# Kernel tuning notes

Measured on AMD Instinct MI355X. Metric: run time of the kernel, lower is better.

## Reference

```python
import jax, jax.numpy as jnp
import numpy as np

UNITS = 512
EPS = 1e-6

def setup_inputs() -> dict:
    key = jax.random.key(0)
    x = jax.random.normal(key, (262144, UNITS), dtype=jnp.float32)
    return {"x": x}

def reference(x):
    d = x.shape[1]
    # Gram matrix with diagonal jitter: [d, d]
    g = x.T @ x + jnp.eye(d, dtype=x.dtype) * EPS
    L = jnp.linalg.cholesky(g)  # lower triangular [d, d]
    # inv(L) via triangular solve (same math as tf.linalg.inv on L)
    L_inv = jax.scipy.linalg.solve_triangular(L, jnp.eye(d, dtype=x.dtype), lower=True)
    ortho_weights = L_inv.T * jnp.sqrt(jnp.float32(UNITS))
    return x @ ortho_weights
```

## Files before the change

### kernel.cpp

```cpp
#include <hip/hip_runtime.h>


#define EPSJ 1e-6f
#define SQRTD 22.627416997969522f

typedef short bf16x8 __attribute__((ext_vector_type(8)));
typedef float f32x4 __attribute__((ext_vector_type(4)));

__device__ __forceinline__ unsigned short f2bf(float f) {
  unsigned u = __float_as_uint(f);
  unsigned r = u + 0x7fffu + ((u >> 16) & 1u);
  return (unsigned short)(r >> 16);
}

__device__ __forceinline__ int swz(int row, int slot) {
  return slot ^ ((row ^ (row >> 3)) & 7);
}

__device__ __forceinline__ float wred(float s) {
  s += __shfl_xor(s, 1);  s += __shfl_xor(s, 2);  s += __shfl_xor(s, 4);
  s += __shfl_xor(s, 8);  s += __shfl_xor(s, 16); s += __shfl_xor(s, 32);
  return s;
}

#define GLOAD16(g, l)                                                         \
  __builtin_amdgcn_global_load_lds(                                           \
      (const __attribute__((address_space(1))) void*)(g),                     \
      (__attribute__((address_space(3))) void*)(l), 16, 0, 0)

__global__ void convert_bf(const float* __restrict__ X,
                           unsigned short* __restrict__ Xbf) {
  long idx = (long)blockIdx.x * blockDim.x + threadIdx.x;
  const long stride = (long)gridDim.x * blockDim.x;
  const long nch = 134217728 / 8;
  for (long i = idx; i < nch; i += stride) {
    float4 f0 = ((const float4*)X)[i * 2];
    float4 f1 = ((const float4*)X)[i * 2 + 1];
    uint4 o;
    o.x = (unsigned)f2bf(f0.x) | ((unsigned)f2bf(f0.y) << 16);
    o.y = (unsigned)f2bf(f0.z) | ((unsigned)f2bf(f0.w) << 16);
    o.z = (unsigned)f2bf(f1.x) | ((unsigned)f2bf(f1.y) << 16);
    o.w = (unsigned)f2bf(f1.z) | ((unsigned)f2bf(f1.w) << 16);
    ((uint4*)Xbf)[i] = o;
  }
}

__device__ __forceinline__ void stage_pack4(
    const unsigned short* __restrict__ src,
    unsigned short* dst, int c0, int kg) {
  uint4 r0 = *(const uint4*)src;
  uint4 r1 = *(const uint4*)(src + 512);
  uint4 r2 = *(const uint4*)(src + 1024);
  uint4 r3 = *(const uint4*)(src + 1536);
  unsigned a[4] = {r0.x, r0.y, r0.z, r0.w};
  unsigned b[4] = {r1.x, r1.y, r1.z, r1.w};
  unsigned c[4] = {r2.x, r2.y, r2.z, r2.w};
  unsigned d[4] = {r3.x, r3.y, r3.z, r3.w};
  const int khi = kg >> 1, koff = (kg & 1) * 8;
  #pragma unroll
  for (int s = 0; s < 8; ++s) {
    int wsel = s >> 1, sh = (s & 1) * 16;
    unsigned v0 = (a[wsel] >> sh) & 0xFFFFu;
    unsigned v1 = (b[wsel] >> sh) & 0xFFFFu;
    unsigned v2 = (c[wsel] >> sh) & 0xFFFFu;
    unsigned v3 = (d[wsel] >> sh) & 0xFFFFu;
    int cc = c0 + s;
    int sl = khi ^ ((cc ^ (cc >> 3)) & 7);
    *(uint2*)((char*)dst + cc * 128 + sl * 16 + koff) =
        make_uint2(v0 | (v1 << 16), v2 | (v3 << 16));
  }
}

__global__ __launch_bounds__(512, 2) void gram_bf(
    const unsigned short* __restrict__ Xbf, float* __restrict__ part,
    int nchunk) {
  __shared__ unsigned short As[256 * 64];
  __shared__ unsigned short Bs[256 * 64];
  const int b = blockIdx.x, pos = b % 3, chunk = b / 3;
  const int s0 = (int)((long)4096 * chunk / nchunk);
  const int s1 = (int)((long)4096 * (chunk + 1) / nchunk);
  const int ca = (pos == 1) ? 256 : 0;
  const int cb2 = (pos == 0) ? 0 : 256;
  const bool diag = (pos != 2);
  const int t = threadIdx.x, lane = t & 63, w = t >> 6;
  const int wr = w >> 2, wc = w & 3;

  f32x4 acc[8][4];
  const f32x4 zf = {0.f, 0.f, 0.f, 0.f};
  #pragma unroll
  for (int a = 0; a < 8; ++a)
    #pragma unroll
    for (int bb = 0; bb < 4; ++bb) acc[a][bb] = zf;

  const int c0 = (t & 31) * 8;
  const int kg = t >> 5;

  for (int ks = s0; ks < s1; ++ks) {
    long r = (long)ks * 64 + kg * 4;
    stage_pack4(Xbf + r * 512 + ca + c0, As, c0, kg);
    if (!diag) stage_pack4(Xbf + r * 512 + cb2 + c0, Bs, c0, kg);
    __syncthreads();
    const unsigned short* Bp = diag ? As : Bs;
    #pragma unroll
    for (int kk = 0; kk < 2; ++kk) {
      bf16x8 af[8], bfr[4];
      #pragma unroll
      for (int fm = 0; fm < 8; ++fm) {
        int row = wr * 128 + fm * 16 + (lane & 15);
        int slot = swz(row, kk * 4 + (lane >> 4));
        af[fm] = *(const bf16x8*)((const char*)As + row * 128 + slot * 16);
      }
      #pragma unroll
      for (int fn = 0; fn < 4; ++fn) {
        int row = wc * 64 + fn * 16 + (lane & 15);
        int slot = swz(row, kk * 4 + (lane >> 4));
        bfr[fn] = *(const bf16x8*)((const char*)Bp + row * 128 + slot * 16);
      }
      #pragma unroll
      for (int fm = 0; fm < 8; ++fm)
        #pragma unroll
        for (int fn = 0; fn < 4; ++fn)
          acc[fm][fn] = __builtin_amdgcn_mfma_f32_16x16x32_bf16(
              bfr[fn], af[fm], acc[fm][fn], 0, 0, 0);
    }
    __syncthreads();
  }
  float* out = part + (long)b * 65536;
  #pragma unroll
  for (int fm = 0; fm < 8; ++fm)
    #pragma unroll
    for (int fn = 0; fn < 4; ++fn) {
      int mi = wr * 128 + fm * 16 + (lane & 15);
      int nj = wc * 64 + fn * 16 + (lane >> 4) * 4;
      *(float4*)(out + mi * 256 + nj) = *(float4*)&acc[fm][fn];
    }
}

__global__ __launch_bounds__(512, 2) void gram_f32(
    const float* __restrict__ X, float* __restrict__ part, int nchunk) {
  __shared__ unsigned short As[256 * 64];
  __shared__ unsigned short Bs[256 * 64];
  const int b = blockIdx.x;
  const int pos = b % 3;
  const int chunk = b / 3;
  const int CR = 262144 / nchunk;
  const long r0 = (long)chunk * CR;
  const int ca = (pos == 1) ? 256 : 0;
  const int cb = (pos == 0) ? 0 : 256;
  const bool diag = (pos != 2);
  const int t = threadIdx.x, lane = t & 63, w = t >> 6;
  const int wr = w >> 2, wc = w & 3;

  f32x4 acc[8][4];
  const f32x4 zf = {0.f, 0.f, 0.f, 0.f};
  #pragma unroll
  for (int a = 0; a < 8; ++a)
    #pragma unroll
    for (int bb = 0; bb < 4; ++bb) acc[a][bb] = zf;

  const int c_oct = t & 31, msub = t >> 5;

  for (int ks = 0; ks < CR; ks += 64) {
    #pragma unroll
    for (int it = 0; it < 4; ++it) {
      int m = msub + 16 * it;
      long row = r0 + ks + m;
      const float4* sa = (const float4*)(X + row * 512 + ca + c_oct * 8);
      float4 a0 = sa[0], a1 = sa[1];
      {
        float v[8] = {a0.x, a0.y, a0.z, a0.w, a1.x, a1.y, a1.z, a1.w};
        #pragma unroll
        for (int s = 0; s < 8; ++s) {
          int cc = c_oct * 8 + s;
          int off = cc * 128 + ((2 * m) ^ (((cc ^ (cc >> 3)) & 7) << 4));
          *(unsigned short*)((char*)As + off) = f2bf(v[s]);
        }
      }
      if (!diag) {
        const float4* sb = (const float4*)(X + row * 512 + cb + c_oct * 8);
        float4 b0 = sb[0], b1 = sb[1];
        float v[8] = {b0.x, b0.y, b0.z, b0.w, b1.x, b1.y, b1.z, b1.w};
        #pragma unroll
        for (int s = 0; s < 8; ++s) {
          int cc = c_oct * 8 + s;
          int off = cc * 128 + ((2 * m) ^ (((cc ^ (cc >> 3)) & 7) << 4));
          *(unsigned short*)((char*)Bs + off) = f2bf(v[s]);
        }
      }
    }
    __syncthreads();
    const unsigned short* Bp = diag ? As : Bs;
    #pragma unroll
    for (int kk = 0; kk < 2; ++kk) {
      bf16x8 af[8], bfr[4];
      #pragma unroll
      for (int fm = 0; fm < 8; ++fm) {
        int row = wr * 128 + fm * 16 + (lane & 15);
        int slot = swz(row, kk * 4 + (lane >> 4));
        af[fm] = *(const bf16x8*)((const char*)As + row * 128 + slot * 16);
      }
      #pragma unroll
      for (int fn = 0; fn < 4; ++fn) {
        int row = wc * 64 + fn * 16 + (lane & 15);
        int slot = swz(row, kk * 4 + (lane >> 4));
        bfr[fn] = *(const bf16x8*)((const char*)Bp + row * 128 + slot * 16);
      }
      #pragma unroll
      for (int fm = 0; fm < 8; ++fm)
        #pragma unroll
        for (int fn = 0; fn < 4; ++fn)
          acc[fm][fn] = __builtin_amdgcn_mfma_f32_16x16x32_bf16(
              bfr[fn], af[fm], acc[fm][fn], 0, 0, 0);
    }
    __syncthreads();
  }
  float* out = part + (long)b * 65536;
  #pragma unroll
  for (int fm = 0; fm < 8; ++fm)
    #pragma unroll
    for (int fn = 0; fn < 4; ++fn) {
      int mi = wr * 128 + fm * 16 + (lane & 15);
      int nj = wc * 64 + fn * 16 + (lane >> 4) * 4;
      *(float4*)(out + mi * 256 + nj) = *(float4*)&acc[fm][fn];
    }
}

__global__ void gram_reduce(const float* __restrict__ part,
                            float* __restrict__ G, int nchunk) {
  int idx = blockIdx.x * 256 + threadIdx.x;
  int pos = idx >> 16;
  int e = idx & 65535;
  float s = 0.f;
  for (int ch = 0; ch < nchunk; ++ch)
    s += part[(long)(ch * 3 + pos) * 65536 + e];
  int i = e >> 8, j = e & 255;
  if (pos == 0) {
    G[i * 512 + j] = s;
  } else if (pos == 1) {
    G[(256 + i) * 512 + 256 + j] = s;
  } else {
    G[i * 512 + 256 + j] = s;
    G[(256 + j) * 512 + i] = s;
  }
}

__global__ __launch_bounds__(256) void chol_step(float* __restrict__ G,
                                                 float* __restrict__ Dinv,
                                                 int p) {
  __shared__ float Pb[64][65];
  __shared__ float Sb[64][65];
  __shared__ float Inv[64][65];
  __shared__ float SbP[64][65];
  __shared__ float Ub[64][65];
  __shared__ float Tt[32][33];
  const int t = threadIdx.x;
  const int r0 = 64 * p;
  const int tr = (t >> 4) * 4, tc = (t & 15) * 4;

  for (int idx = t; idx < 4096; idx += 256) {
    int i = idx >> 6, j = idx & 63;
    float v = G[(long)(r0 + i) * 512 + r0 + j];
    if (i == j) v += EPSJ;
    Pb[i][j] = v;
  }
  __syncthreads();

  if (p > 0) {
    float cc[4][4] = {{0.f}};
    for (int r = 0; r < p; ++r) {
      for (int idx = t; idx < 4096; idx += 256) {
        int i = idx >> 6, j = idx & 63;
        Sb[i][j] = G[(long)(r0 + i) * 512 + 64 * r + j];
      }
      __syncthreads();
      #pragma unroll 4
      for (int k = 0; k < 64; ++k) {
        float a0 = Sb[tr][k], a1 = Sb[tr+1][k], a2 = Sb[tr+2][k], a3 = Sb[tr+3][k];
        float b0 = Sb[tc][k], b1 = Sb[tc+1][k], b2 = Sb[tc+2][k], b3 = Sb[tc+3][k];
        cc[0][0]+=a0*b0; cc[0][1]+=a0*b1; cc[0][2]+=a0*b2; cc[0][3]+=a0*b3;
        cc[1][0]+=a1*b0; cc[1][1]+=a1*b1; cc[1][2]+=a1*b2; cc[1][3]+=a1*b3;
        cc[2][0]+=a2*b0; cc[2][1]+=a2*b1; cc[2][2]+=a2*b2; cc[2][3]+=a2*b3;
        cc[3][0]+=a3*b0; cc[3][1]+=a3*b1; cc[3][2]+=a3*b2; cc[3][3]+=a3*b3;
      }
      __syncthreads();
    }
    #pragma unroll
    for (int u = 0; u < 4; ++u)
      #pragma unroll
      for (int v = 0; v < 4; ++v)
        Pb[tr + u][tc + v] -= cc[u][v];
    __syncthreads();
  }

  const int lane = t & 63, w = t >> 6;
  #pragma unroll
  for (int sp = 0; sp < 2; ++sp) {
    const int b0 = sp * 32;
    if (w == 0) {
      float rr[32];
      #pragma unroll
      for (int k = 0; k < 32; ++k)
        rr[k] = (lane < 32) ? Pb[b0 + lane][b0 + k] : 0.f;
      #pragma unroll
      for (int j = 0; j < 32; ++j) {
        float d = sqrtf(__shfl(rr[j], j));
        if (lane == j) rr[j] = d;
        else if (lane > j && lane < 32) rr[j] = rr[j] / d;
        float rj = rr[j];
        #pragma unroll
        for (int k = j + 1; k < 32; ++k) {
          float Lkj = __shfl(rj, k);
          if (lane > j && lane < 32) rr[k] -= rj * Lkj;
        }
      }
      #pragma unroll
      for (int k = 0; k < 32; ++k)
        if (lane < 32) Pb[b0 + lane][b0 + k] = rr[k];
    }
    __syncthreads();
    if (sp == 0) {
      if (t < 32) {
        int rw = 32 + t;
        float x[32];
        #pragma unroll
        for (int j = 0; j < 32; ++j) x[j] = Pb[rw][j];
        #pragma unroll
        for (int j = 0; j < 32; ++j) {
          float xj = x[j] / Pb[j][j];
          x[j] = xj;
          #pragma unroll
          for (int k2 = j + 1; k2 < 32; ++k2) x[k2] -= xj * Pb[k2][j];
        }
        #pragma unroll
        for (int j = 0; j < 32; ++j) Pb[rw][j] = x[j];
      }
      __syncthreads();
      {
        int i = 32 + (t >> 3), kb = 32 + (t & 7) * 4;
        float sv[4];
        #pragma unroll
        for (int e = 0; e < 4; ++e) sv[e] = Pb[i][kb + e];
        #pragma unroll 4
        for (int j = 0; j < 32; ++j) {
          float aij = Pb[i][j];
          #pragma unroll
          for (int e = 0; e < 4; ++e) sv[e] -= aij * Pb[kb + e][j];
        }
        #pragma unroll
        for (int e = 0; e < 4; ++e) Pb[i][kb + e] = sv[e];
      }
      __syncthreads();
    }
  }

  if (t < 64) {
    int col = t & 31, o = (t >> 5) * 32;
    float x[32];
    #pragma unroll
    for (int i = 0; i < 32; ++i) {
      float s = (i == col) ? 1.f : 0.f;
      #pragma unroll
      for (int j = 0; j < i; ++j) s -= Pb[o + i][o + j] * x[j];
      x[i] = s / Pb[o + i][o + i];
    }
    #pragma unroll
    for (int i = 0; i < 32; ++i) Inv[o + i][o + col] = x[i];
  }
  for (int idx = t; idx < 1024; idx += 256)
    Inv[idx >> 5][32 + (idx & 31)] = 0.f;
  __syncthreads();
  {
    int i = t >> 3, jb = (t & 7) * 4;
    float sv[4] = {0.f, 0.f, 0.f, 0.f};
    #pragma unroll 4
    for (int k = 0; k < 32; ++k) {
      float bik = Pb[32 + i][k];
      #pragma unroll
      for (int e = 0; e < 4; ++e) sv[e] += bik * Inv[k][jb + e];
    }
    #pragma unroll
    for (int e = 0; e < 4; ++e) Tt[i][jb + e] = sv[e];
  }
  __syncthreads();
  {
    int i = t >> 3, jb = (t & 7) * 4;
    float sv[4] = {0.f, 0.f, 0.f, 0.f};
    #pragma unroll 4
    for (int k = 0; k < 32; ++k) {
      float cik = Inv[32 + i][32 + k];
      #pragma unroll
      for (int e = 0; e < 4; ++e) sv[e] += cik * Tt[k][jb + e];
    }
    #pragma unroll
    for (int e = 0; e < 4; ++e) Inv[32 + i][jb + e] = -sv[e];
  }
  __syncthreads();

  if (blockIdx.x == 0) {
    for (int idx = t; idx < 4096; idx += 256)
      Dinv[p * 4096 + idx] = Inv[idx >> 6][idx & 63];
    return;
  }

  const long rI = 64 * (p + blockIdx.x), cP = 64 * p;
  float cc2[4][4] = {{0.f}};
  for (int r = 0; r < p; ++r) {
    __syncthreads();
    for (int idx = t; idx < 4096; idx += 256) {
      int i = idx >> 6, j = idx & 63;
      Sb[i][j] = G[(rI + i) * 512 + 64 * r + j];
      SbP[i][j] = G[(cP + i) * 512 + 64 * r + j];
    }
    __syncthreads();
    #pragma unroll 4
    for (int k = 0; k < 64; ++k) {
      float a0 = Sb[tr][k], a1 = Sb[tr+1][k], a2 = Sb[tr+2][k], a3 = Sb[tr+3][k];
      float b0 = SbP[tc][k], b1 = SbP[tc+1][k], b2 = SbP[tc+2][k], b3 = SbP[tc+3][k];
      cc2[0][0]+=a0*b0; cc2[0][1]+=a0*b1; cc2[0][2]+=a0*b2; cc2[0][3]+=a0*b3;
      cc2[1][0]+=a1*b0; cc2[1][1]+=a1*b1; cc2[1][2]+=a1*b2; cc2[1][3]+=a1*b3;
      cc2[2][0]+=a2*b0; cc2[2][1]+=a2*b1; cc2[2][2]+=a2*b2; cc2[2][3]+=a2*b3;
      cc2[3][0]+=a3*b0; cc2[3][1]+=a3*b1; cc2[3][2]+=a3*b2; cc2[3][3]+=a3*b3;
    }
  }
  __syncthreads();
  #pragma unroll
  for (int u = 0; u < 4; ++u)
    #pragma unroll
    for (int v = 0; v < 4; ++v)
      Ub[tr + u][tc + v] = G[(rI + tr + u) * 512 + cP + tc + v] - cc2[u][v];
  __syncthreads();
  float xx[4][4] = {{0.f}};
  #pragma unroll 4
  for (int k = 0; k < 64; ++k) {
    float a0 = Ub[tr][k], a1 = Ub[tr+1][k], a2 = Ub[tr+2][k], a3 = Ub[tr+3][k];
    float b0 = Inv[tc][k], b1 = Inv[tc+1][k], b2 = Inv[tc+2][k], b3 = Inv[tc+3][k];
    xx[0][0]+=a0*b0; xx[0][1]+=a0*b1; xx[0][2]+=a0*b2; xx[0][3]+=a0*b3;
    xx[1][0]+=a1*b0; xx[1][1]+=a1*b1; xx[1][2]+=a1*b2; xx[1][3]+=a1*b3;
    xx[2][0]+=a2*b0; xx[2][1]+=a2*b1; xx[2][2]+=a2*b2; xx[2][3]+=a2*b3;
    xx[3][0]+=a3*b0; xx[3][1]+=a3*b1; xx[3][2]+=a3*b2; xx[3][3]+=a3*b3;
  }
  #pragma unroll
  for (int u = 0; u < 4; ++u)
    #pragma unroll
    for (int v = 0; v < 4; ++v)
      G[(rI + tr + u) * 512 + cP + tc + v] = xx[u][v];
}

__global__ __launch_bounds__(256) void tri_assemble(
    const float* __restrict__ G, const float* __restrict__ Dinv,
    unsigned short* __restrict__ Wt) {
  __shared__ float Bsh[448 * 64];
  __shared__ float T[64 * 64];
  const int q = blockIdx.x, t = threadIdx.x;
  const int or_ = (t >> 4) * 4, oc = (t & 15) * 4;

  for (int p = q + 1; p < 8; ++p) {
    float cc[4][4] = {{0.f}};
    for (int r = q; r < p; ++r) {
      const float* Lbase = G + (long)(64 * p) * 512 + 64 * r;
      #pragma unroll 4
      for (int k = 0; k < 64; ++k) {
        float a0 = Lbase[(or_ + 0) * 512 + k];
        float a1 = Lbase[(or_ + 1) * 512 + k];
        float a2 = Lbase[(or_ + 2) * 512 + k];
        float a3 = Lbase[(or_ + 3) * 512 + k];
        float b0, b1, b2, b3;
        if (r == q) {
          const float* Bq = Dinv + q * 4096 + k * 64 + oc;
          b0 = Bq[0]; b1 = Bq[1]; b2 = Bq[2]; b3 = Bq[3];
        } else {
          const float* Br = Bsh + ((r - q - 1) * 64 + k) * 64 + oc;
          b0 = Br[0]; b1 = Br[1]; b2 = Br[2]; b3 = Br[3];
        }
        cc[0][0] += a0*b0; cc[0][1] += a0*b1; cc[0][2] += a0*b2; cc[0][3] += a0*b3;
        cc[1][0] += a1*b0; cc[1][1] += a1*b1; cc[1][2] += a1*b2; cc[1][3] += a1*b3;
        cc[2][0] += a2*b0; cc[2][1] += a2*b1; cc[2][2] += a2*b2; cc[2][3] += a2*b3;
        cc[3][0] += a3*b0; cc[3][1] += a3*b1; cc[3][2] += a3*b2; cc[3][3] += a3*b3;
      }
    }
    #pragma unroll
    for (int u = 0; u < 4; ++u)
      #pragma unroll
      for (int v = 0; v < 4; ++v)
        T[(or_ + u) * 64 + oc + v] = cc[u][v];
    __syncthreads();

    float c2[4][4] = {{0.f}};
    const float* Dp = Dinv + p * 4096;
    #pragma unroll 4
    for (int k = 0; k < 64; ++k) {
      float a0 = Dp[(or_ + 0) * 64 + k];
      float a1 = Dp[(or_ + 1) * 64 + k];
      float a2 = Dp[(or_ + 2) * 64 + k];
      float a3 = Dp[(or_ + 3) * 64 + k];
      const float* Tk = T + k * 64 + oc;
      float b0 = Tk[0], b1 = Tk[1], b2 = Tk[2], b3 = Tk[3];
      c2[0][0] += a0*b0; c2[0][1] += a0*b1; c2[0][2] += a0*b2; c2[0][3] += a0*b3;
      c2[1][0] += a1*b0; c2[1][1] += a1*b1; c2[1][2] += a1*b2; c2[1][3] += a1*b3;
      c2[2][0] += a2*b0; c2[2][1] += a2*b1; c2[2][2] += a2*b2; c2[2][3] += a2*b3;
      c2[3][0] += a3*b0; c2[3][1] += a3*b1; c2[3][2] += a3*b2; c2[3][3] += a3*b3;
    }
    #pragma unroll
    for (int u = 0; u < 4; ++u)
      #pragma unroll
      for (int v = 0; v < 4; ++v)
        Bsh[((p - q - 1) * 64 + or_ + u) * 64 + oc + v] = -c2[u][v];
    __syncthreads();
  }

  const int nr = (8 - q) * 64;
  for (int idx = t; idx < nr * 64; idx += 256) {
    int i = idx >> 6, kk = idx & 63;
    float v = (i < 64) ? Dinv[q * 4096 + i * 64 + kk]
                       : Bsh[(i - 64) * 64 + kk];
    int n = 64 * q + i;
    Wt[(long)n * 512 + 64 * q + kk] = f2bf(SQRTD * v);
  }
  for (int idx = t; idx < 64 * q * 64; idx += 256) {
    int n = idx >> 6, kk = idx & 63;
    Wt[(long)n * 512 + 64 * q + kk] = 0;
  }
}

__global__ __launch_bounds__(512, 4) void ymm7(
    const unsigned short* __restrict__ Xbf,
    const unsigned short* __restrict__ Wt, float* __restrict__ Y) {
  __shared__ unsigned short As[2][128 * 64];
  __shared__ unsigned short Bs[2][128 * 64];
  const int t = threadIdx.x, lane = t & 63, w = t >> 6;
  const int id = blockIdx.x;
  const int xcd = id & 7, j = id >> 3;
  const long m0 = (long)((j >> 2) * 8 + xcd) * 128;
  const int n0 = (j & 3) * 128;
  const int wm = (w >> 1) * 32, wn = (w & 1) * 64;
  f32x4 acc[2][4];
  const f32x4 zf = {0.f, 0.f, 0.f, 0.f};
  #pragma unroll
  for (int a = 0; a < 2; ++a)
    #pragma unroll
    for (int bq = 0; bq < 4; ++bq) acc[a][bq] = zf;

  auto stage = [&](int buf, int k0) {
    #pragma unroll
    for (int h = 0; h < 2; ++h) {
      int seg = t + h * 512;
      int row = seg >> 3, sl = seg & 7;
      const unsigned short* sA =
          Xbf + (m0 + row) * 512 + k0 + swz(row, sl) * 8;
      const unsigned short* sB =
          Wt + (long)(n0 + row) * 512 + k0 + swz(row, sl) * 8;
      GLOAD16(sA, &As[buf][seg * 8]);
      GLOAD16(sB, &Bs[buf][seg * 8]);
    }
  };
  auto compute = [&](int buf) {
    #pragma unroll
    for (int kk = 0; kk < 2; ++kk) {
      bf16x8 af[2], bfr[4];
      #pragma unroll
      for (int fm = 0; fm < 2; ++fm) {
        int row = wm + fm * 16 + (lane & 15);
        af[fm] = *(const bf16x8*)((const char*)As[buf] + row * 128 +
                                  swz(row, kk * 4 + (lane >> 4)) * 16);
      }
      #pragma unroll
      for (int fn = 0; fn < 4; ++fn) {
        int row = wn + fn * 16 + (lane & 15);
        bfr[fn] = *(const bf16x8*)((const char*)Bs[buf] + row * 128 +
                                   swz(row, kk * 4 + (lane >> 4)) * 16);
      }
      #pragma unroll
      for (int fm = 0; fm < 2; ++fm)
        #pragma unroll
        for (int fn = 0; fn < 4; ++fn)
          acc[fm][fn] = __builtin_amdgcn_mfma_f32_16x16x32_bf16(
              bfr[fn], af[fm], acc[fm][fn], 0, 0, 0);
    }
  };

  stage(0, 0);
  asm volatile("s_waitcnt vmcnt(0)" ::: "memory");
  __builtin_amdgcn_s_barrier();
  int cur = 0;
  #pragma unroll 1
  for (int kt = 0; kt < 7; ++kt) {
    stage(cur ^ 1, (kt + 1) * 64);
    asm volatile("s_waitcnt vmcnt(4)" ::: "memory");
    __builtin_amdgcn_s_barrier();
    compute(cur);
    asm volatile("s_waitcnt lgkmcnt(0)" ::: "memory");
    __builtin_amdgcn_s_barrier();
    cur ^= 1;
  }
  asm volatile("s_waitcnt vmcnt(0)" ::: "memory");
  __builtin_amdgcn_s_barrier();
  compute(cur);

  #pragma unroll
  for (int fm = 0; fm < 2; ++fm)
    #pragma unroll
    for (int fn = 0; fn < 4; ++fn) {
      long row = m0 + wm + fm * 16 + (lane & 15);
      int col = n0 + wn + fn * 16 + (lane >> 4) * 4;
      *(float4*)(Y + row * 512 + col) = *(float4*)&acc[fm][fn];
    }
}

__global__ __launch_bounds__(256) void ymm_v1(const float* __restrict__ X,
                                              const unsigned short* __restrict__ Wt,
                                              float* __restrict__ Y) {
  __shared__ unsigned short As[128 * 64];
  __shared__ unsigned short Bs[128 * 64];
  const int t = threadIdx.x, lane = t & 63, w = t >> 6;
  const long m0 = (long)blockIdx.x * 128;
  const int n0 = blockIdx.y * 128;
  const int wm = (w >> 1) * 64, wn = (w & 1) * 64;
  f32x4 acc[4][4];
  const f32x4 zf = {0.f, 0.f, 0.f, 0.f};
  #pragma unroll
  for (int a = 0; a < 4; ++a)
    #pragma unroll
    for (int bq = 0; bq < 4; ++bq) acc[a][bq] = zf;
  const int ko = t & 7, mrow = t >> 3;

  for (int k0 = 0; k0 < 512; k0 += 64) {
    #pragma unroll
    for (int it = 0; it < 4; ++it) {
      int m = mrow + 32 * it;
      const float4* src = (const float4*)(X + (m0 + m) * 512 + k0 + ko * 8);
      float4 f0 = src[0], f1 = src[1];
      unsigned p0 = (unsigned)f2bf(f0.x) | ((unsigned)f2bf(f0.y) << 16);
      unsigned p1 = (unsigned)f2bf(f0.z) | ((unsigned)f2bf(f0.w) << 16);
      unsigned p2 = (unsigned)f2bf(f1.x) | ((unsigned)f2bf(f1.y) << 16);
      unsigned p3 = (unsigned)f2bf(f1.z) | ((unsigned)f2bf(f1.w) << 16);
      int slot = swz(m, ko);
      *(uint4*)((char*)As + m * 128 + slot * 16) = make_uint4(p0, p1, p2, p3);
    }
    #pragma unroll
    for (int it = 0; it < 4; ++it) {
      int n = mrow + 32 * it;
      uint4 raw = *(const uint4*)(Wt + (long)(n0 + n) * 512 + k0 + ko * 8);
      int slot = swz(n, ko);
      *(uint4*)((char*)Bs + n * 128 + slot * 16) = raw;
    }
    __syncthreads();
    #pragma unroll
    for (int kk = 0; kk < 2; ++kk) {
      bf16x8 af[4], bfr[4];
      #pragma unroll
      for (int fm = 0; fm < 4; ++fm) {
        int row = wm + fm * 16 + (lane & 15);
        af[fm] = *(const bf16x8*)((const char*)As + row * 128 +
                                  swz(row, kk * 4 + (lane >> 4)) * 16);
      }
      #pragma unroll
      for (int fn = 0; fn < 4; ++fn) {
        int row = wn + fn * 16 + (lane & 15);
        bfr[fn] = *(const bf16x8*)((const char*)Bs + row * 128 +
                                   swz(row, kk * 4 + (lane >> 4)) * 16);
      }
      #pragma unroll
      for (int fm = 0; fm < 4; ++fm)
        #pragma unroll
        for (int fn = 0; fn < 4; ++fn)
          acc[fm][fn] = __builtin_amdgcn_mfma_f32_16x16x32_bf16(
              af[fm], bfr[fn], acc[fm][fn], 0, 0, 0);
    }
    __syncthreads();
  }
  #pragma unroll
  for (int fm = 0; fm < 4; ++fm)
    #pragma unroll
    for (int fn = 0; fn < 4; ++fn)
      #pragma unroll
      for (int j = 0; j < 4; ++j) {
        long row = m0 + wm + fm * 16 + (lane >> 4) * 4 + j;
        int col = n0 + wn + fn * 16 + (lane & 15);
        Y[row * 512 + col] = acc[fm][fn][j];
      }
}

extern "C" void kernel_launch(void* const* d_in, const int* in_sizes, int n_in,
                              void* d_out, int out_size, void* d_ws, size_t ws_size,
                              hipStream_t stream) {
  const float* X = (const float*)d_in[0];
  float* Y = (float*)d_out;
  char* ws = (char*)d_ws;
  float* G = (float*)ws;
  unsigned short* Wt = (unsigned short*)(ws + (1 << 20));
  float* Dinv = (float*)(ws + (1 << 20) + (1 << 19));

  const int NCH_FAST = 85;
  size_t part_off = (size_t)(2 << 20);
  size_t part_bytes = (size_t)NCH_FAST * 3 * 65536 * 4;
  size_t xbf_off = part_off + part_bytes;
  size_t need = xbf_off + (size_t)134217728 * 2;

  if (ws_size >= need) {
    float* part = (float*)(ws + part_off);
    unsigned short* Xbf = (unsigned short*)(ws + xbf_off);
    convert_bf<<<2048, 256, 0, stream>>>(X, Xbf);
    gram_bf<<<3 * NCH_FAST, 512, 0, stream>>>(Xbf, part, NCH_FAST);
    gram_reduce<<<768, 256, 0, stream>>>(part, G, NCH_FAST);
    for (int p = 0; p < 8; ++p)
      chol_step<<<8 - p, 256, 0, stream>>>(G, Dinv, p);
    tri_assemble<<<8, 256, 0, stream>>>(G, Dinv, Wt);
    ymm7<<<8192, 512, 0, stream>>>(Xbf, Wt, Y);
  } else {
    float* part = (float*)(ws + part_off);
    size_t fixed = part_off;
    int nchunk = 64;
    while (nchunk > 1 && fixed + (size_t)nchunk * 3 * 65536 * 4 > ws_size)
      nchunk >>= 1;
    gram_f32<<<3 * nchunk, 512, 0, stream>>>(X, part, nchunk);
    gram_reduce<<<768, 256, 0, stream>>>(part, G, nchunk);
    for (int p = 0; p < 8; ++p)
      chol_step<<<8 - p, 256, 0, stream>>>(G, Dinv, p);
    tri_assemble<<<8, 256, 0, stream>>>(G, Dinv, Wt);
    ymm_v1<<<dim3(2048, 4), 256, 0, stream>>>(X, Wt, Y);
  }
}
```

Before: 1.458 ms.

## Fuse Cholesky steps and triangular assembly into one persistent kernel with grid barriers

Replaces the eight per-panel chol_step launches and the separate tri_assemble launch with a single 8-block persistent kernel. The blocks synchronise between panel stages through atomic-counter grid barriers, using flags that gram_reduce zeroes. This removes about eight kernel launches and their gaps from the serial Cholesky chain. In exchange it relies on all 8 blocks being co-resident and on spin-waiting, and it adds fence and atomic latency at every stage.

```diff
diff --git a/kernel.cpp b/kernel.cpp
--- a/kernel.cpp
+++ b/kernel.cpp
@@ -17,16 +17,22 @@
   return slot ^ ((row ^ (row >> 3)) & 7);
 }
 
-__device__ __forceinline__ float wred(float s) {
-  s += __shfl_xor(s, 1);  s += __shfl_xor(s, 2);  s += __shfl_xor(s, 4);
-  s += __shfl_xor(s, 8);  s += __shfl_xor(s, 16); s += __shfl_xor(s, 32);
-  return s;
-}
-
 #define GLOAD16(g, l)                                                         \
   __builtin_amdgcn_global_load_lds(                                           \
       (const __attribute__((address_space(1))) void*)(g),                     \
       (__attribute__((address_space(3))) void*)(l), 16, 0, 0)
+
+__device__ __forceinline__ void gbar(unsigned* f) {
+  __syncthreads();
+  if (threadIdx.x == 0) {
+    __threadfence();
+    atomicAdd(f, 1u);
+    while (__hip_atomic_load(f, __ATOMIC_ACQUIRE, __HIP_MEMORY_SCOPE_AGENT) <
+           8u) {
+    }
+  }
+  __syncthreads();
+}
 
 __global__ void convert_bf(const float* __restrict__ X,
                            unsigned short* __restrict__ Xbf) {
@@ -226,7 +232,9 @@
 }
 
 __global__ void gram_reduce(const float* __restrict__ part,
-                            float* __restrict__ G, int nchunk) {
+                            float* __restrict__ G, unsigned* __restrict__ flags,
+                            int nchunk) {
+  if (blockIdx.x == 0 && threadIdx.x < 32) flags[threadIdx.x] = 0u;
   int idx = blockIdx.x * 256 + threadIdx.x;
   int pos = idx >> 16;
   int e = idx & 65535;
@@ -244,215 +252,198 @@
   }
 }
 
-__global__ __launch_bounds__(256) void chol_step(float* __restrict__ G,
+__global__ __launch_bounds__(256) void chol_mono(float* __restrict__ G,
                                                  float* __restrict__ Dinv,
-                                                 int p) {
-  __shared__ float Pb[64][65];
-  __shared__ float Sb[64][65];
-  __shared__ float Inv[64][65];
-  __shared__ float SbP[64][65];
-  __shared__ float Ub[64][65];
-  __shared__ float Tt[32][33];
-  const int t = threadIdx.x;
-  const int r0 = 64 * p;
+                                                 unsigned short* __restrict__ Wt,
+                                                 unsigned* __restrict__ flags) {
+  __shared__ __align__(16) char smraw[131072];
+  float* SbI = (float*)smraw;
+  float* SbP = SbI + 4160;
+  float* W1  = SbP + 4160;
+  float* Inv = W1 + 4160;
+  float* Tt  = Inv + 4160;
+  const int b = blockIdx.x, t = threadIdx.x;
   const int tr = (t >> 4) * 4, tc = (t & 15) * 4;
-
-  for (int idx = t; idx < 4096; idx += 256) {
-    int i = idx >> 6, j = idx & 63;
-    float v = G[(long)(r0 + i) * 512 + r0 + j];
-    if (i == j) v += EPSJ;
-    Pb[i][j] = v;
-  }
-  __syncthreads();
-
-  if (p > 0) {
+  const int lane = t & 63, w = t >> 6;
+
+  for (int p = 0; p < 8; ++p) {
+    if (b < p) { gbar(flags + 2 * p); gbar(flags + 2 * p + 1); continue; }
+    const long rI = 64 * b, cP = 64 * p;
     float cc[4][4] = {{0.f}};
     for (int r = 0; r < p; ++r) {
+      __syncthreads();
       for (int idx = t; idx < 4096; idx += 256) {
-        int i = idx >> 6, j = idx & 63;
-        Sb[i][j] = G[(long)(r0 + i) * 512 + 64 * r + j];
+        int i = idx >> 6, jj = idx & 63;
+        SbI[i * 65 + jj] = G[(rI + i) * 512 + 64 * r + jj];
+        SbP[i * 65 + jj] = G[(cP + i) * 512 + 64 * r + jj];
       }
       __syncthreads();
       #pragma unroll 4
       for (int k = 0; k < 64; ++k) {
-        float a0 = Sb[tr][k], a1 = Sb[tr+1][k], a2 = Sb[tr+2][k], a3 = Sb[tr+3][k];
-        float b0 = Sb[tc][k], b1 = Sb[tc+1][k], b2 = Sb[tc+2][k], b3 = Sb[tc+3][k];
+        float a0 = SbI[(tr+0)*65+k], a1 = SbI[(tr+1)*65+k];
+        float a2 = SbI[(tr+2)*65+k], a3 = SbI[(tr+3)*65+k];
+        float b0 = SbP[(tc+0)*65+k], b1 = SbP[(tc+1)*65+k];
+        float b2 = SbP[(tc+2)*65+k], b3 = SbP[(tc+3)*65+k];
         cc[0][0]+=a0*b0; cc[0][1]+=a0*b1; cc[0][2]+=a0*b2; cc[0][3]+=a0*b3;
         cc[1][0]+=a1*b0; cc[1][1]+=a1*b1; cc[1][2]+=a1*b2; cc[1][3]+=a1*b3;
         cc[2][0]+=a2*b0; cc[2][1]+=a2*b1; cc[2][2]+=a2*b2; cc[2][3]+=a2*b3;
         cc[3][0]+=a3*b0; cc[3][1]+=a3*b1; cc[3][2]+=a3*b2; cc[3][3]+=a3*b3;
       }
+    }
+    __syncthreads();
+    if (b == p) {
+      #pragma unroll
+      for (int u = 0; u < 4; ++u)
+        #pragma unroll
+        for (int v = 0; v < 4; ++v) {
+          int i = tr + u, jj = tc + v;
+          float vv = G[(cP + i) * 512 + cP + jj] - cc[u][v];
+          if (i == jj) vv += EPSJ;
+          W1[i * 65 + jj] = vv;
+        }
       __syncthreads();
-    }
-    #pragma unroll
-    for (int u = 0; u < 4; ++u)
-      #pragma unroll
-      for (int v = 0; v < 4; ++v)
-        Pb[tr + u][tc + v] -= cc[u][v];
-    __syncthreads();
-  }
-
-  const int lane = t & 63, w = t >> 6;
-  #pragma unroll
-  for (int sp = 0; sp < 2; ++sp) {
-    const int b0 = sp * 32;
-    if (w == 0) {
-      float rr[32];
-      #pragma unroll
-      for (int k = 0; k < 32; ++k)
-        rr[k] = (lane < 32) ? Pb[b0 + lane][b0 + k] : 0.f;
-      #pragma unroll
-      for (int j = 0; j < 32; ++j) {
-        float d = sqrtf(__shfl(rr[j], j));
-        if (lane == j) rr[j] = d;
-        else if (lane > j && lane < 32) rr[j] = rr[j] / d;
-        float rj = rr[j];
-        #pragma unroll
-        for (int k = j + 1; k < 32; ++k) {
-          float Lkj = __shfl(rj, k);
-          if (lane > j && lane < 32) rr[k] -= rj * Lkj;
-        }
-      }
-      #pragma unroll
-      for (int k = 0; k < 32; ++k)
-        if (lane < 32) Pb[b0 + lane][b0 + k] = rr[k];
-    }
-    __syncthreads();
-    if (sp == 0) {
-      if (t < 32) {
-        int rw = 32 + t;
+      #pragma unroll
+      for (int sp = 0; sp < 2; ++sp) {
+        const int b0 = sp * 32;
+        if (w == 0) {
+          float rr[32];
+          #pragma unroll
+          for (int k = 0; k < 32; ++k)
+            rr[k] = (lane < 32) ? W1[(b0 + lane) * 65 + b0 + k] : 0.f;
+          #pragma unroll
+          for (int j = 0; j < 32; ++j) {
+            float d = sqrtf(__shfl(rr[j], j));
+            if (lane == j) rr[j] = d;
+            else if (lane > j && lane < 32) rr[j] = rr[j] / d;
+            float rj = rr[j];
+            #pragma unroll
+            for (int k = j + 1; k < 32; ++k) {
+              float Lkj = __shfl(rj, k);
+              if (lane > j && lane < 32) rr[k] -= rj * Lkj;
+            }
+          }
+          #pragma unroll
+          for (int k = 0; k < 32; ++k)
+            if (lane < 32) W1[(b0 + lane) * 65 + b0 + k] = rr[k];
+        }
+        __syncthreads();
+        if (sp == 0) {
+          if (t < 32) {
+            int rw = 32 + t;
+            float x[32];
+            #pragma unroll
+            for (int j = 0; j < 32; ++j) x[j] = W1[rw * 65 + j];
+            #pragma unroll
+            for (int j = 0; j < 32; ++j) {
+              float xj = x[j] / W1[j * 65 + j];
+              x[j] = xj;
+              #pragma unroll
+              for (int k2 = j + 1; k2 < 32; ++k2) x[k2] -= xj * W1[k2 * 65 + j];
+            }
+            #pragma unroll
+            for (int j = 0; j < 32; ++j) W1[rw * 65 + j] = x[j];
+          }
+          __syncthreads();
+          {
+            int i = 32 + (t >> 3), kb = 32 + (t & 7) * 4;
+            float sv[4];
+            #pragma unroll
+            for (int e = 0; e < 4; ++e) sv[e] = W1[i * 65 + kb + e];
+            #pragma unroll 4
+            for (int j = 0; j < 32; ++j) {
+              float aij = W1[i * 65 + j];
+              #pragma unroll
+              for (int e = 0; e < 4; ++e) sv[e] -= aij * W1[(kb + e) * 65 + j];
+            }
+            #pragma unroll
+            for (int e = 0; e < 4; ++e) W1[i * 65 + kb + e] = sv[e];
+          }
+          __syncthreads();
+        }
+      }
+      if (t < 64) {
+        int col = t & 31, o = (t >> 5) * 32;
         float x[32];
         #pragma unroll
-        for (int j = 0; j < 32; ++j) x[j] = Pb[rw][j];
-        #pragma unroll
-        for (int j = 0; j < 32; ++j) {
-          float xj = x[j] / Pb[j][j];
-          x[j] = xj;
+        for (int i = 0; i < 32; ++i) {
+          float s = (i == col) ? 1.f : 0.f;
           #pragma unroll
-          for (int k2 = j + 1; k2 < 32; ++k2) x[k2] -= xj * Pb[k2][j];
-        }
-        #pragma unroll
-        for (int j = 0; j < 32; ++j) Pb[rw][j] = x[j];
-      }
+          for (int j = 0; j < i; ++j) s -= W1[(o + i) * 65 + o + j] * x[j];
+          x[i] = s / W1[(o + i) * 65 + o + i];
+        }
+        #pragma unroll
+        for (int i = 0; i < 32; ++i) Inv[(o + i) * 65 + o + col] = x[i];
+      }
+      for (int idx = t; idx < 1024; idx += 256)
+        Inv[(idx >> 5) * 65 + 32 + (idx & 31)] = 0.f;
       __syncthreads();
       {
-        int i = 32 + (t >> 3), kb = 32 + (t & 7) * 4;
-        float sv[4];
-        #pragma unroll
-        for (int e = 0; e < 4; ++e) sv[e] = Pb[i][kb + e];
+        int i = t >> 3, jb = (t & 7) * 4;
+        float sv[4] = {0.f, 0.f, 0.f, 0.f};
         #pragma unroll 4
-        for (int j = 0; j < 32; ++j) {
-          float aij = Pb[i][j];
+        for (int k = 0; k < 32; ++k) {
+          float bik = W1[(32 + i) * 65 + k];
           #pragma unroll
-          for (int e = 0; e < 4; ++e) sv[e] -= aij * Pb[kb + e][j];
-        }
-        #pragma unroll
-        for (int e = 0; e < 4; ++e) Pb[i][kb + e] = sv[e];
+          for (int e = 0; e < 4; ++e) sv[e] += bik * Inv[k * 65 + jb + e];
+        }
+        #pragma unroll
+        for (int e = 0; e < 4; ++e) Tt[i * 33 + jb + e] = sv[e];
       }
       __syncthreads();
-    }
-  }
-
-  if (t < 64) {
-    int col = t & 31, o = (t >> 5) * 32;
-    float x[32];
-    #pragma unroll
-    for (int i = 0; i < 32; ++i) {
-      float s = (i == col) ? 1.f : 0.f;
-      #pragma unroll
-      for (int j = 0; j < i; ++j) s -= Pb[o + i][o + j] * x[j];
-      x[i] = s / Pb[o + i][o + i];
-    }
-    #pragma unroll
-    for (int i = 0; i < 32; ++i) Inv[o + i][o + col] = x[i];
-  }
-  for (int idx = t; idx < 1024; idx += 256)
-    Inv[idx >> 5][32 + (idx & 31)] = 0.f;
+      {
+        int i = t >> 3, jb = (t & 7) * 4;
+        float sv[4] = {0.f, 0.f, 0.f, 0.f};
+        #pragma unroll 4
+        for (int k = 0; k < 32; ++k) {
+          float cik = Inv[(32 + i) * 65 + 32 + k];
+          #pragma unroll
+          for (int e = 0; e < 4; ++e) sv[e] += cik * Tt[k * 33 + jb + e];
+        }
+        #pragma unroll
+        for (int e = 0; e < 4; ++e) Inv[(32 + i) * 65 + jb + e] = -sv[e];
+      }
+      __syncthreads();
+      for (int idx = t; idx < 4096; idx += 256)
+        Dinv[p * 4096 + idx] = Inv[(idx >> 6) * 65 + (idx & 63)];
+    } else {
+      #pragma unroll
+      for (int u = 0; u < 4; ++u)
+        #pragma unroll
+        for (int v = 0; v < 4; ++v)
+          W1[(tr + u) * 65 + tc + v] =
+              G[(rI + tr + u) * 512 + cP + tc + v] - cc[u][v];
+    }
+    gbar(flags + 2 * p);
+    if (b > p) {
+      for (int idx = t; idx < 4096; idx += 256)
+        Inv[(idx >> 6) * 65 + (idx & 63)] = Dinv[p * 4096 + idx];
+      __syncthreads();
+      float xx[4][4] = {{0.f}};
+      #pragma unroll 4
+      for (int k = 0; k < 64; ++k) {
+        float a0 = W1[(tr+0)*65+k], a1 = W1[(tr+1)*65+k];
+        float a2 = W1[(tr+2)*65+k], a3 = W1[(tr+3)*65+k];
+        float b0 = Inv[(tc+0)*65+k], b1 = Inv[(tc+1)*65+k];
+        float b2 = Inv[(tc+2)*65+k], b3 = Inv[(tc+3)*65+k];
+        xx[0][0]+=a0*b0; xx[0][1]+=a0*b1; xx[0][2]+=a0*b2; xx[0][3]+=a0*b3;
+        xx[1][0]+=a1*b0; xx[1][1]+=a1*b1; xx[1][2]+=a1*b2; xx[1][3]+=a1*b3;
+        xx[2][0]+=a2*b0; xx[2][1]+=a2*b1; xx[2][2]+=a2*b2; xx[2][3]+=a2*b3;
+        xx[3][0]+=a3*b0; xx[3][1]+=a3*b1; xx[3][2]+=a3*b2; xx[3][3]+=a3*b3;
+      }
+      #pragma unroll
+      for (int u = 0; u < 4; ++u)
+        #pragma unroll
+        for (int v = 0; v < 4; ++v)
+          G[(rI + tr + u) * 512 + cP + tc + v] = xx[u][v];
+    }
+    gbar(flags + 2 * p + 1);
+  }
+
+  float* Bsh = (float*)smraw;
+  float* T = Bsh + 28672;
+  const int q = b;
+  const int or_ = (t >> 4) * 4, oc = (t & 15) * 4;
   __syncthreads();
-  {
-    int i = t >> 3, jb = (t & 7) * 4;
-    float sv[4] = {0.f, 0.f, 0.f, 0.f};
-    #pragma unroll 4
-    for (int k = 0; k < 32; ++k) {
-      float bik = Pb[32 + i][k];
-      #pragma unroll
-      for (int e = 0; e < 4; ++e) sv[e] += bik * Inv[k][jb + e];
-    }
-    #pragma unroll
-    for (int e = 0; e < 4; ++e) Tt[i][jb + e] = sv[e];
-  }
-  __syncthreads();
-  {
-    int i = t >> 3, jb = (t & 7) * 4;
-    float sv[4] = {0.f, 0.f, 0.f, 0.f};
-    #pragma unroll 4
-    for (int k = 0; k < 32; ++k) {
-      float cik = Inv[32 + i][32 + k];
-      #pragma unroll
-      for (int e = 0; e < 4; ++e) sv[e] += cik * Tt[k][jb + e];
-    }
-    #pragma unroll
-    for (int e = 0; e < 4; ++e) Inv[32 + i][jb + e] = -sv[e];
-  }
-  __syncthreads();
-
-  if (blockIdx.x == 0) {
-    for (int idx = t; idx < 4096; idx += 256)
-      Dinv[p * 4096 + idx] = Inv[idx >> 6][idx & 63];
-    return;
-  }
-
-  const long rI = 64 * (p + blockIdx.x), cP = 64 * p;
-  float cc2[4][4] = {{0.f}};
-  for (int r = 0; r < p; ++r) {
-    __syncthreads();
-    for (int idx = t; idx < 4096; idx += 256) {
-      int i = idx >> 6, j = idx & 63;
-      Sb[i][j] = G[(rI + i) * 512 + 64 * r + j];
-      SbP[i][j] = G[(cP + i) * 512 + 64 * r + j];
-    }
-    __syncthreads();
-    #pragma unroll 4
-    for (int k = 0; k < 64; ++k) {
-      float a0 = Sb[tr][k], a1 = Sb[tr+1][k], a2 = Sb[tr+2][k], a3 = Sb[tr+3][k];
-      float b0 = SbP[tc][k], b1 = SbP[tc+1][k], b2 = SbP[tc+2][k], b3 = SbP[tc+3][k];
-      cc2[0][0]+=a0*b0; cc2[0][1]+=a0*b1; cc2[0][2]+=a0*b2; cc2[0][3]+=a0*b3;
-      cc2[1][0]+=a1*b0; cc2[1][1]+=a1*b1; cc2[1][2]+=a1*b2; cc2[1][3]+=a1*b3;
-      cc2[2][0]+=a2*b0; cc2[2][1]+=a2*b1; cc2[2][2]+=a2*b2; cc2[2][3]+=a2*b3;
-      cc2[3][0]+=a3*b0; cc2[3][1]+=a3*b1; cc2[3][2]+=a3*b2; cc2[3][3]+=a3*b3;
-    }
-  }
-  __syncthreads();
-  #pragma unroll
-  for (int u = 0; u < 4; ++u)
-    #pragma unroll
-    for (int v = 0; v < 4; ++v)
-      Ub[tr + u][tc + v] = G[(rI + tr + u) * 512 + cP + tc + v] - cc2[u][v];
-  __syncthreads();
-  float xx[4][4] = {{0.f}};
-  #pragma unroll 4
-  for (int k = 0; k < 64; ++k) {
-    float a0 = Ub[tr][k], a1 = Ub[tr+1][k], a2 = Ub[tr+2][k], a3 = Ub[tr+3][k];
-    float b0 = Inv[tc][k], b1 = Inv[tc+1][k], b2 = Inv[tc+2][k], b3 = Inv[tc+3][k];
-    xx[0][0]+=a0*b0; xx[0][1]+=a0*b1; xx[0][2]+=a0*b2; xx[0][3]+=a0*b3;
-    xx[1][0]+=a1*b0; xx[1][1]+=a1*b1; xx[1][2]+=a1*b2; xx[1][3]+=a1*b3;
-    xx[2][0]+=a2*b0; xx[2][1]+=a2*b1; xx[2][2]+=a2*b2; xx[2][3]+=a2*b3;
-    xx[3][0]+=a3*b0; xx[3][1]+=a3*b1; xx[3][2]+=a3*b2; xx[3][3]+=a3*b3;
-  }
-  #pragma unroll
-  for (int u = 0; u < 4; ++u)
-    #pragma unroll
-    for (int v = 0; v < 4; ++v)
-      G[(rI + tr + u) * 512 + cP + tc + v] = xx[u][v];
-}
-
-__global__ __launch_bounds__(256) void tri_assemble(
-    const float* __restrict__ G, const float* __restrict__ Dinv,
-    unsigned short* __restrict__ Wt) {
-  __shared__ float Bsh[448 * 64];
-  __shared__ float T[64 * 64];
-  const int q = blockIdx.x, t = threadIdx.x;
-  const int or_ = (t >> 4) * 4, oc = (t & 15) * 4;
 
   for (int p = q + 1; p < 8; ++p) {
     float cc[4][4] = {{0.f}};
@@ -689,6 +680,7 @@
   float* G = (float*)ws;
   unsigned short* Wt = (unsigned short*)(ws + (1 << 20));
   float* Dinv = (float*)(ws + (1 << 20) + (1 << 19));
+  unsigned* flags = (unsigned*)(ws + (7 << 18));
 
   const int NCH_FAST = 85;
   size_t part_off = (size_t)(2 << 20);
@@ -701,10 +693,8 @@
     unsigned short* Xbf = (unsigned short*)(ws + xbf_off);
     convert_bf<<<2048, 256, 0, stream>>>(X, Xbf);
     gram_bf<<<3 * NCH_FAST, 512, 0, stream>>>(Xbf, part, NCH_FAST);
-    gram_reduce<<<768, 256, 0, stream>>>(part, G, NCH_FAST);
-    for (int p = 0; p < 8; ++p)
-      chol_step<<<8 - p, 256, 0, stream>>>(G, Dinv, p);
-    tri_assemble<<<8, 256, 0, stream>>>(G, Dinv, Wt);
+    gram_reduce<<<768, 256, 0, stream>>>(part, G, flags, NCH_FAST);
+    chol_mono<<<8, 256, 0, stream>>>(G, Dinv, Wt, flags);
     ymm7<<<8192, 512, 0, stream>>>(Xbf, Wt, Y);
   } else {
     float* part = (float*)(ws + part_off);
@@ -713,10 +703,8 @@
     while (nchunk > 1 && fixed + (size_t)nchunk * 3 * 65536 * 4 > ws_size)
       nchunk >>= 1;
     gram_f32<<<3 * nchunk, 512, 0, stream>>>(X, part, nchunk);
-    gram_reduce<<<768, 256, 0, stream>>>(part, G, nchunk);
-    for (int p = 0; p < 8; ++p)
-      chol_step<<<8 - p, 256, 0, stream>>>(G, Dinv, p);
-    tri_assemble<<<8, 256, 0, stream>>>(G, Dinv, Wt);
+    gram_reduce<<<768, 256, 0, stream>>>(part, G, flags, nchunk);
+    chol_mono<<<8, 256, 0, stream>>>(G, Dinv, Wt, flags);
     ymm_v1<<<dim3(2048, 4), 256, 0, stream>>>(X, Wt, Y);
   }
 }
```

After: 1.450 ms. Within noise of the previous version (-0.5%).
